# Kernel tuning notes

Measured on AMD Instinct MI355X. Metric: run time of the kernel, lower is better.

Reference implementation:

```python
import jax, jax.numpy as jnp
import numpy as np

N = 100000; E = 1600000; D_IN = 9; HID = 16; HEADS = 8; D = HID * HEADS; G = 1000
NEG_SLOPE = 0.2; LN_EPS = 1e-5


def _gat_conv(x, src, dst, W, a_src, a_dst, b, heads, ch):
    # PyG GATConv (eval mode, self-loops already appended to src/dst)
    h = (x @ W).reshape(-1, heads, ch)                   # [N,H,C]
    al_s = (h * a_src).sum(-1)                           # [N,H]
    al_d = (h * a_dst).sum(-1)                           # [N,H]
    e = al_s[src] + al_d[dst]                            # [Et,H]
    e = jnp.where(e > 0, e, NEG_SLOPE * e)               # LeakyReLU(0.2)
    m = jax.ops.segment_max(e, dst, num_segments=N)      # per-dst softmax
    alpha = jnp.exp(e - m[dst])
    denom = jax.ops.segment_sum(alpha, dst, num_segments=N)
    alpha = alpha / (denom[dst] + 1e-16)
    out = jax.ops.segment_sum(h[src] * alpha[:, :, None], dst, num_segments=N)
    return out.reshape(-1, heads * ch) + b


def _ln_graph(x, g, b):
    # PyG LayerNorm, mode='graph', batch=None: normalize over all nodes+channels
    mu = x.mean()
    var = jnp.mean((x - mu) ** 2)
    return (x - mu) / jnp.sqrt(var + LN_EPS) * g + b


def setup_inputs() -> dict:
    key = jax.random.key(0)
    ks = jax.random.split(key, 20)
    s = 0.1
    p = lambda i, shape: jax.random.normal(ks[i], shape, jnp.float32) * s
    return {
        "x": jax.random.normal(ks[0], (N, D_IN), jnp.float32),
        "edge_index": jax.random.randint(ks[1], (2, E), 0, N),
        "batch": jnp.sort(jax.random.randint(ks[2], (N,), 0, G)),
        "W1": p(3, (D_IN, D)), "a_src1": p(4, (HEADS, HID)), "a_dst1": p(5, (HEADS, HID)), "b1": jnp.zeros((D,), jnp.float32),
        "W2": p(6, (D, D)), "a_src2": p(7, (1, D)), "a_dst2": p(8, (1, D)), "b2": jnp.zeros((D,), jnp.float32),
        "fc1_w": p(9, (D, D)), "fc1_b": jnp.zeros((D,), jnp.float32),
        "fc2_w": p(10, (D, D)), "fc2_b": jnp.zeros((D,), jnp.float32),
        "fc3_w": p(11, (D, D)), "fc3_b": jnp.zeros((D,), jnp.float32),
        "fc4_w": p(12, (D, D)), "fc4_b": jnp.zeros((D,), jnp.float32),
        "g1": jnp.ones((D,), jnp.float32), "beta1": jnp.zeros((D,), jnp.float32),
        "g2": jnp.ones((D,), jnp.float32), "beta2": jnp.zeros((D,), jnp.float32),
        "fcf_w": p(13, (D, 1)), "fcf_b": jnp.zeros((1,), jnp.float32),
    }


def reference(x, edge_index, batch, W1, a_src1, a_dst1, b1, W2, a_src2, a_dst2, b2,
              fc1_w, fc1_b, fc2_w, fc2_b, fc3_w, fc3_b, fc4_w, fc4_b,
              g1, beta1, g2, beta2, fcf_w, fcf_b):
    loops = jnp.arange(N)
    src = jnp.concatenate([edge_index[0], loops])
    dst = jnp.concatenate([edge_index[1], loops])
    h = jax.nn.relu(_gat_conv(x, src, dst, W1, a_src1, a_dst1, b1, HEADS, HID))
    hc = h
    h = jax.nn.relu(h @ fc1_w + fc1_b)
    h = jax.nn.relu(h @ fc2_w + fc2_b + hc)
    h = _ln_graph(h, g1, beta1)
    hc = h
    h = _gat_conv(h, src, dst, W2, a_src2, a_dst2, b2, 1, D)
    h = jax.nn.relu(h @ fc3_w + fc3_b)
    h = h @ fc4_w + fc4_b + hc
    h = _ln_graph(h, g2, beta2)
    h = h @ fcf_w + fcf_b                                # [N,1]
    sums = jax.ops.segment_sum(h, batch, num_segments=G)
    cnt = jax.ops.segment_sum(jnp.ones((N,), h.dtype), batch, num_segments=G)
    return sums / jnp.maximum(cnt, 1.0)[:, None]          # global_mean_pool -> [G,1]
```

## Files before the change

kernel.cpp:

```cpp
#include <hip/hip_runtime.h>
#include <cstdint>

#define NN 100000
#define NE 1600000
#define DI 9
#define DD 128
#define NH 8
#define NG 1000

#define NBK 3125
#define NBLK 256
#define EPB (NE/NBLK)

typedef unsigned int uint;
typedef __attribute__((ext_vector_type(8))) short bf16x8;
typedef __attribute__((ext_vector_type(4))) float f32x4;

__device__ __forceinline__ float leaky(float x){ return x > 0.f ? x : 0.2f*x; }
__device__ __forceinline__ uint f2bf(float f){
  uint u = __float_as_uint(f);
  return (u + 0x7fffu + ((u>>16)&1u)) >> 16;
}
__device__ __forceinline__ float bflo(uint p){ return __uint_as_float(p << 16); }
__device__ __forceinline__ float bfhi(uint p){ return __uint_as_float(p & 0xffff0000u); }
__device__ __forceinline__ uint packbf(float a, float b){ return f2bf(a) | (f2bf(b)<<16); }

union U16 { uint4 u; bf16x8 v; };
__device__ __forceinline__ bf16x8 ld8(const uint* p){ U16 t; t.u = *(const uint4*)p; return t.v; }

__global__ __launch_bounds__(512) void k_hist(const int* __restrict__ dst, int* __restrict__ hist){
  __shared__ int h[NBK];
  for (int i = threadIdx.x; i < NBK; i += 512) h[i] = 0;
  __syncthreads();
  int blk = blockIdx.x;
  int beg = blk*EPB, end = beg + EPB;
  for (int i = beg + threadIdx.x; i < end; i += 512)
    atomicAdd(&h[dst[i] >> 5], 1);
  __syncthreads();
  for (int b = threadIdx.x; b < NBK; b += 512) hist[(size_t)blk*NBK + b] = h[b];
}

__global__ __launch_bounds__(256) void k_bsum(int* __restrict__ hist, int* __restrict__ bsum){
  int b = blockIdx.x*256 + threadIdx.x;
  if (b >= NBK) return;
  int run = 0;
  for (int k = 0; k < NBLK; ++k){
    int t = hist[(size_t)k*NBK + b];
    hist[(size_t)k*NBK + b] = run;
    run += t;
  }
  bsum[b] = run;
}

__global__ __launch_bounds__(1024) void k_bscan(const int* __restrict__ bsum, int* __restrict__ bbase){
  __shared__ int sh[1024];
  __shared__ int carry;
  if (threadIdx.x == 0) carry = 0;
  __syncthreads();
  for (int c0 = 0; c0 < NBK; c0 += 1024){
    int i = c0 + threadIdx.x;
    int v = (i < NBK) ? bsum[i] : 0;
    sh[threadIdx.x] = v;
    __syncthreads();
    for (int off = 1; off < 1024; off <<= 1){
      int t = (threadIdx.x >= off) ? sh[threadIdx.x-off] : 0;
      __syncthreads();
      sh[threadIdx.x] += t;
      __syncthreads();
    }
    if (i < NBK) bbase[i] = carry + sh[threadIdx.x] - v;
    __syncthreads();
    if (threadIdx.x == 0) carry += sh[1023];
    __syncthreads();
  }
}

__global__ __launch_bounds__(512) void k_part(const int* __restrict__ src, const int* __restrict__ dst,
    const int* __restrict__ hist, const int* __restrict__ bbase, uint* __restrict__ ebuf){
  __shared__ int cur[NBK];
  int blk = blockIdx.x;
  for (int b = threadIdx.x; b < NBK; b += 512)
    cur[b] = hist[(size_t)blk*NBK + b] + bbase[b];
  __syncthreads();
  int beg = blk*EPB, end = beg + EPB;
  for (int i = beg + threadIdx.x; i < end; i += 512){
    int d = dst[i], s = src[i];
    int b = d >> 5;
    int p = atomicAdd(&cur[b], 1);
    ebuf[p] = (uint)s | ((uint)(d & 31) << 26);
  }
}

__global__ __launch_bounds__(64) void k_fin(const uint* __restrict__ ebuf, const int* __restrict__ bbase,
    const int* __restrict__ bsum, int* __restrict__ rowptr, int* __restrict__ col){
  __shared__ int cnt32[32];
  __shared__ int exc[32];
  int b = blockIdx.x;
  int lane = threadIdx.x;
  if (lane < 32) cnt32[lane] = 0;
  __syncthreads();
  int base = bbase[b], n = bsum[b];
  for (int i = lane; i < n; i += 64)
    atomicAdd(&cnt32[ebuf[base+i] >> 26], 1);
  __syncthreads();
  if (lane == 0){
    int run = 0;
    for (int d = 0; d < 32; ++d){
      int t = cnt32[d];
      exc[d] = run;
      rowptr[b*32 + d] = base + run;
      run += t;
    }
  }
  __syncthreads();
  if (lane < 32) cnt32[lane] = exc[lane];
  __syncthreads();
  for (int i = lane; i < n; i += 64){
    uint e = ebuf[base+i];
    int d = e >> 26;
    int r = atomicAdd(&cnt32[d], 1);
    col[base + r] = (int)(e & 0x03ffffffu);
  }
  if (b == 0 && lane == 0) rowptr[NN] = NE;
}

__global__ __launch_bounds__(64) void k_wconv5(const float* __restrict__ w0, const float* __restrict__ w1,
    const float* __restrict__ w2, const float* __restrict__ w3, const float* __restrict__ w4,
    uint* __restrict__ o0, uint* __restrict__ o1, uint* __restrict__ o2,
    uint* __restrict__ o3, uint* __restrict__ o4){
  int which = blockIdx.x >> 7;
  int n = blockIdx.x & 127;
  int t = threadIdx.x;
  const float* W = (which==0)?w0:(which==1)?w1:(which==2)?w2:(which==3)?w3:w4;
  uint* WT = (which==0)?o0:(which==1)?o1:(which==2)?o2:(which==3)?o3:o4;
  float a = W[(2*t)*DD + n];
  float b = W[(2*t+1)*DD + n];
  WT[n*64 + t] = packbf(a, b);
}

__global__ __launch_bounds__(128) void k_lin1(const float* __restrict__ x, const float* __restrict__ W1,
    const float* __restrict__ as1, const float* __restrict__ ad1,
    uint* __restrict__ t1b, float* __restrict__ al_s, float* __restrict__ al_d){
  int n = blockIdx.x;
  int c = threadIdx.x;
  const float* xr = x + n*DI;
  float t = 0.f;
  #pragma unroll
  for (int k = 0; k < DI; ++k) t = fmaf(xr[k], W1[k*DD+c], t);
  uint mybf = f2bf(t);
  uint pbf  = (uint)__shfl_xor((int)mybf, 1, 64);
  if (!(c & 1)) t1b[(size_t)n*64 + (c>>1)] = mybf | (pbf<<16);
  float vs = t * as1[c];
  float vd = t * ad1[c];
  #pragma unroll
  for (int m = 8; m >= 1; m >>= 1){ vs += __shfl_xor(vs, m, 16); vd += __shfl_xor(vd, m, 16); }
  if ((c & 15) == 0){
    al_s[n*NH + (c>>4)] = vs;
    al_d[n*NH + (c>>4)] = vd;
  }
}

__global__ __launch_bounds__(256) void k_gat1(const uint* __restrict__ t1b,
    const float* __restrict__ al_s, const float* __restrict__ al_d,
    const int* __restrict__ rowptr, const int* __restrict__ col,
    const float* __restrict__ b1, uint* __restrict__ outb){
  int n = blockIdx.x*4 + (threadIdx.x >> 6);
  if (n >= NN) return;
  uint lane = threadIdx.x & 63;
  uint h = lane >> 3;
  float ald = al_d[(uint)n*NH + h];
  float a0  = __expf(leaky(al_s[(uint)n*NH + h] + ald));
  uint  ps  = t1b[(uint)n*64u + lane];
  float den = a0;
  float s0 = a0*bflo(ps), s1 = a0*bfhi(ps);
  int beg = rowptr[n], end = rowptr[n+1];
  for (int e = beg; e < end; e += 16){
    uint cs[16]; float ls[16]; uint pp[16];
    #pragma unroll
    for (int j = 0; j < 16; ++j){
      int ej = e + j;
      cs[j] = (uint)col[(ej < end) ? ej : (end-1)];
    }
    #pragma unroll
    for (int j = 0; j < 16; ++j){
      ls[j] = al_s[cs[j]*8u + h];
      pp[j] = t1b[cs[j]*64u + lane];
    }
    #pragma unroll
    for (int j = 0; j < 16; ++j){
      float a = (e + j < end) ? __expf(leaky(ls[j] + ald)) : 0.f;
      den += a;
      s0 = fmaf(a, bflo(pp[j]), s0);
      s1 = fmaf(a, bfhi(pp[j]), s1);
    }
  }
  float inv = 1.f/(den + 1e-16f);
  float2 bb = ((const float2*)b1)[lane];
  outb[(uint)n*64u + lane] = packbf(fmaxf(s0*inv + bb.x, 0.f), fmaxf(s1*inv + bb.y, 0.f));
}

__global__ __launch_bounds__(256) void k_gat2(const uint* __restrict__ t2b,
    const float* __restrict__ al_s, const float* __restrict__ al_d,
    const int* __restrict__ rowptr, const int* __restrict__ col,
    const float* __restrict__ b2, uint* __restrict__ outb){
  int n = blockIdx.x*4 + (threadIdx.x >> 6);
  if (n >= NN) return;
  uint lane = threadIdx.x & 63;
  float ald = al_d[n];
  float a0  = __expf(leaky(al_s[n] + ald));
  uint  ps  = t2b[(uint)n*64u + lane];
  float den = a0;
  float s0 = a0*bflo(ps), s1 = a0*bfhi(ps);
  int beg = rowptr[n], end = rowptr[n+1];
  for (int e = beg; e < end; e += 16){
    uint cs[16]; float ls[16]; uint pp[16];
    #pragma unroll
    for (int j = 0; j < 16; ++j){
      int ej = e + j;
      cs[j] = (uint)col[(ej < end) ? ej : (end-1)];
    }
    #pragma unroll
    for (int j = 0; j < 16; ++j){
      ls[j] = al_s[cs[j]];
      pp[j] = t2b[cs[j]*64u + lane];
    }
    #pragma unroll
    for (int j = 0; j < 16; ++j){
      float a = (e + j < end) ? __expf(leaky(ls[j] + ald)) : 0.f;
      den += a;
      s0 = fmaf(a, bflo(pp[j]), s0);
      s1 = fmaf(a, bfhi(pp[j]), s1);
    }
  }
  float inv = 1.f/(den + 1e-16f);
  float2 bb = ((const float2*)b2)[lane];
  outb[(uint)n*64u + lane] = packbf(s0*inv + bb.x, s1*inv + bb.y);
}

template<bool RELU, bool BIAS, bool RES, bool LNRED, bool AL2>
__global__ __launch_bounds__(256) void k_mfma(const uint* __restrict__ Xb, const uint* __restrict__ WTb,
    const float* __restrict__ bias, const uint* __restrict__ resb, uint* __restrict__ outb,
    float* __restrict__ pbuf, const float* __restrict__ avs, const float* __restrict__ avd,
    float* __restrict__ o_als, float* __restrict__ o_ald, int nrows){
  int lane = threadIdx.x & 63;
  int wid  = threadIdx.x >> 6;
  int m0 = blockIdx.x*128 + wid*32;
  int lr = lane & 15, hi4 = lane >> 4;
  f32x4 acc[2][8];
  #pragma unroll
  for (int a = 0; a < 2; ++a)
    #pragma unroll
    for (int c = 0; c < 8; ++c) acc[a][c] = (f32x4){0.f,0.f,0.f,0.f};
  int ra0 = m0 + lr;      if (ra0 > NN-1) ra0 = NN-1;
  int ra1 = m0 + 16 + lr; if (ra1 > NN-1) ra1 = NN-1;
  #pragma unroll
  for (int kk = 0; kk < 4; ++kk){
    int ko = kk*16 + hi4*4;
    bf16x8 a0 = ld8(Xb + (size_t)ra0*64 + ko);
    bf16x8 a1 = ld8(Xb + (size_t)ra1*64 + ko);
    #pragma unroll
    for (int c = 0; c < 8; ++c){
      bf16x8 b = ld8(WTb + (size_t)(c*16 + lr)*64 + ko);
      acc[0][c] = __builtin_amdgcn_mfma_f32_16x16x32_bf16(a0, b, acc[0][c], 0, 0, 0);
      acc[1][c] = __builtin_amdgcn_mfma_f32_16x16x32_bf16(a1, b, acc[1][c], 0, 0, 0);
    }
  }
  if (AL2){
    #pragma unroll
    for (int rg = 0; rg < 2; ++rg){
      #pragma unroll
      for (int r = 0; r < 4; ++r){
        float vs = 0.f, vd = 0.f;
        #pragma unroll
        for (int c = 0; c < 8; ++c){
          float v = acc[rg][c][r];
          vs = fmaf(v, avs[c*16 + lr], vs);
          vd = fmaf(v, avd[c*16 + lr], vd);
        }
        #pragma unroll
        for (int m = 8; m >= 1; m >>= 1){ vs += __shfl_xor(vs, m, 64); vd += __shfl_xor(vd, m, 64); }
        int row = m0 + rg*16 + hi4*4 + r;
        if (lr == 0 && row < nrows){ o_als[row] = vs; o_ald[row] = vd; }
      }
    }
  }
  bool evn = !(lane & 1);
  int cph = lr >> 1;
  float lns = 0.f, lnss = 0.f;
  #pragma unroll
  for (int rg = 0; rg < 2; ++rg){
    #pragma unroll
    for (int c = 0; c < 8; ++c){
      int cp = c*8 + cph;
      #pragma unroll
      for (int r = 0; r < 4; ++r){
        float v0 = acc[rg][c][r];
        float v1 = __shfl_xor(v0, 1, 64);
        int row = m0 + rg*16 + hi4*4 + r;
        if (evn && row < nrows){
          if (BIAS){ float2 bb = ((const float2*)bias)[cp]; v0 += bb.x; v1 += bb.y; }
          if (RES){ uint rr = resb[(size_t)row*64 + cp]; v0 += bflo(rr); v1 += bfhi(rr); }
          if (RELU){ v0 = fmaxf(v0, 0.f); v1 = fmaxf(v1, 0.f); }
          outb[(size_t)row*64 + cp] = packbf(v0, v1);
          if (LNRED){ lns += v0 + v1; lnss += v0*v0 + v1*v1; }
        }
      }
    }
  }
  if (LNRED){
    #pragma unroll
    for (int m = 32; m >= 1; m >>= 1){ lns += __shfl_xor(lns, m, 64); lnss += __shfl_xor(lnss, m, 64); }
    __shared__ float shred[8];
    if (lane == 0){ shred[wid*2] = lns; shred[wid*2+1] = lnss; }
    __syncthreads();
    if (threadIdx.x == 0){
      float S = 0.f, SS = 0.f;
      for (int w = 0; w < 4; ++w){ S += shred[2*w]; SS += shred[2*w+1]; }
      pbuf[blockIdx.x*2] = S; pbuf[blockIdx.x*2+1] = SS;
    }
  }
}

__global__ __launch_bounds__(256) void k_ln_stats(const float* __restrict__ pbuf, float* __restrict__ stats, int nb){
  float s = 0.f, ss = 0.f;
  for (int i = threadIdx.x; i < nb; i += 256){ s += pbuf[2*i]; ss += pbuf[2*i+1]; }
  #pragma unroll
  for (int m = 32; m >= 1; m >>= 1){ s += __shfl_xor(s, m, 64); ss += __shfl_xor(ss, m, 64); }
  __shared__ float sh[8];
  int wid = threadIdx.x >> 6, lane = threadIdx.x & 63;
  if (lane == 0){ sh[wid*2] = s; sh[wid*2+1] = ss; }
  __syncthreads();
  if (threadIdx.x == 0){
    float S = 0.f, SS = 0.f;
    for (int w = 0; w < 4; ++w){ S += sh[2*w]; SS += sh[2*w+1]; }
    const float inv = 1.f/((float)NN*(float)DD);
    float mu = S*inv;
    float var = SS*inv - mu*mu;
    stats[0] = mu;
    stats[1] = rsqrtf(var + 1e-5f);
  }
}

__global__ __launch_bounds__(256) void k_ln_apply_bf(uint* __restrict__ xb, const float* __restrict__ g,
    const float* __restrict__ be, const float* __restrict__ stats){
  const int n4 = NN*16;
  float mu = stats[0], rs = stats[1];
  uint4* x4 = (uint4*)xb;
  const float2* g2 = (const float2*)g;
  const float2* b2 = (const float2*)be;
  for (int i = blockIdx.x*256 + threadIdx.x; i < n4; i += gridDim.x*256){
    int cb = (i & 15)*4;
    uint4 u = x4[i];
    float2 ga = g2[cb],   gb = g2[cb+1], gc = g2[cb+2], gd = g2[cb+3];
    float2 ba = b2[cb],   bb = b2[cb+1], bc = b2[cb+2], bd = b2[cb+3];
    u.x = packbf((bflo(u.x)-mu)*rs*ga.x + ba.x, (bfhi(u.x)-mu)*rs*ga.y + ba.y);
    u.y = packbf((bflo(u.y)-mu)*rs*gb.x + bb.x, (bfhi(u.y)-mu)*rs*gb.y + bb.y);
    u.z = packbf((bflo(u.z)-mu)*rs*gc.x + bc.x, (bfhi(u.z)-mu)*rs*gc.y + bc.y);
    u.w = packbf((bflo(u.w)-mu)*rs*gd.x + bd.x, (bfhi(u.w)-mu)*rs*gd.y + bd.y);
    x4[i] = u;
  }
}

__global__ __launch_bounds__(256) void k_fdot_ln(const uint* __restrict__ xb, const float* __restrict__ g,
    const float* __restrict__ be, const float* __restrict__ stats,
    const float* __restrict__ fw, const float* __restrict__ fb, float* __restrict__ val){
  int n = blockIdx.x*4 + (threadIdx.x >> 6);
  if (n >= NN) return;
  int lane = threadIdx.x & 63;
  float mu = stats[0], rs = stats[1];
  uint p = xb[(size_t)n*64 + lane];
  float2 gg = ((const float2*)g)[lane];
  float2 bb = ((const float2*)be)[lane];
  float2 ww = ((const float2*)fw)[lane];
  float v = ((bflo(p)-mu)*rs*gg.x + bb.x)*ww.x + ((bfhi(p)-mu)*rs*gg.y + bb.y)*ww.y;
  #pragma unroll
  for (int m = 32; m >= 1; m >>= 1) v += __shfl_xor(v, m, 64);
  if (lane == 0) val[n] = v + fb[0];
}

__global__ __launch_bounds__(64) void k_pool(const float* __restrict__ val, const int* __restrict__ batch,
                                             float* __restrict__ out){
  int g = blockIdx.x;
  int lane = threadIdx.x;
  int lo = 0, hi = NN;
  while (lo < hi){ int mid = (lo+hi)>>1; if (batch[mid] < g) lo = mid+1; else hi = mid; }
  int start = lo;
  hi = NN;
  while (lo < hi){ int mid = (lo+hi)>>1; if (batch[mid] < g+1) lo = mid+1; else hi = mid; }
  int end = lo;
  float s = 0.f;
  for (int i = start + lane; i < end; i += 64) s += val[i];
  #pragma unroll
  for (int m = 32; m >= 1; m >>= 1) s += __shfl_xor(s, m, 64);
  if (lane == 0) out[g] = s / fmaxf((float)(end - start), 1.f);
}

extern "C" void kernel_launch(void* const* d_in, const int* in_sizes, int n_in,
                              void* d_out, int out_size, void* d_ws, size_t ws_size,
                              hipStream_t stream){
  const float* x   = (const float*)d_in[0];
  const int*   ei  = (const int*)d_in[1];
  const int* batch = (const int*)d_in[2];
  const float* W1  = (const float*)d_in[3];
  const float* as1 = (const float*)d_in[4];
  const float* ad1 = (const float*)d_in[5];
  const float* b1  = (const float*)d_in[6];
  const float* W2  = (const float*)d_in[7];
  const float* as2 = (const float*)d_in[8];
  const float* ad2 = (const float*)d_in[9];
  const float* b2  = (const float*)d_in[10];
  const float* fc1w= (const float*)d_in[11];
  const float* fc1b= (const float*)d_in[12];
  const float* fc2w= (const float*)d_in[13];
  const float* fc2b= (const float*)d_in[14];
  const float* fc3w= (const float*)d_in[15];
  const float* fc3b= (const float*)d_in[16];
  const float* fc4w= (const float*)d_in[17];
  const float* fc4b= (const float*)d_in[18];
  const float* g1  = (const float*)d_in[19];
  const float* be1 = (const float*)d_in[20];
  const float* g2  = (const float*)d_in[21];
  const float* be2 = (const float*)d_in[22];
  const float* fcw = (const float*)d_in[23];
  const float* fcb = (const float*)d_in[24];
  float* out = (float*)d_out;
  (void)in_sizes; (void)n_in; (void)out_size; (void)ws_size;

  char* ws = (char*)d_ws;
  size_t off = 0;
  auto alloc = [&](size_t bytes)->void*{
    void* p = ws + off;
    off += (bytes + 255) & ~(size_t)255;
    return p;
  };
  float* A    = (float*)alloc((size_t)NN*DD*4);
  float* B    = (float*)alloc((size_t)NN*DD*4);
  float* C    = (float*)alloc((size_t)NN*DD*4);
  float* als1 = (float*)alloc((size_t)NN*NH*4);
  float* ald1 = (float*)alloc((size_t)NN*NH*4);
  float* als2 = (float*)alloc((size_t)NN*4);
  float* ald2 = (float*)alloc((size_t)NN*4);
  float* escr = (float*)alloc((size_t)NE*4);
  int*   rowptr = (int*)alloc((size_t)(NN+1)*4);
  int*   col    = (int*)alloc((size_t)NE*4);
  int*   bsum   = (int*)alloc((size_t)NBK*4);
  int*   bbase  = (int*)alloc((size_t)NBK*4);
  float* pbuf   = (float*)alloc(1024*2*4);
  float* stats  = (float*)alloc(2*4);
  float* val    = (float*)alloc((size_t)NN*4);
  uint* wt_fc1  = (uint*)alloc((size_t)DD*64*4);
  uint* wt_fc2  = (uint*)alloc((size_t)DD*64*4);
  uint* wt_w2   = (uint*)alloc((size_t)DD*64*4);
  uint* wt_fc3  = (uint*)alloc((size_t)DD*64*4);
  uint* wt_fc4  = (uint*)alloc((size_t)DD*64*4);

  uint*  Ab     = (uint*)A;
  uint*  Bb     = (uint*)B;
  uint*  Cb     = (uint*)C;
  int*   hist   = (int*)A;
  uint*  ebuf   = (uint*)escr;

  const int* esrc = ei;
  const int* edst = ei + NE;

  k_hist <<<NBLK, 512, 0, stream>>>(edst, hist);
  k_bsum <<<(NBK+255)/256, 256, 0, stream>>>(hist, bsum);
  k_bscan<<<1, 1024, 0, stream>>>(bsum, bbase);
  k_part <<<NBLK, 512, 0, stream>>>(esrc, edst, hist, bbase, ebuf);
  k_fin  <<<NBK, 64, 0, stream>>>(ebuf, bbase, bsum, rowptr, col);

  k_wconv5<<<5*DD, 64, 0, stream>>>(fc1w, fc2w, W2, fc3w, fc4w,
                                    wt_fc1, wt_fc2, wt_w2, wt_fc3, wt_fc4);

  const int WB = (NN + 3)/4;
  const int GB = (NN + 127)/128;

  k_lin1<<<NN, 128, 0, stream>>>(x, W1, as1, ad1, Ab, als1, ald1);
  k_gat1<<<WB, 256, 0, stream>>>(Ab, als1, ald1, rowptr, col, b1, Bb);

  k_mfma<true,  true, false, false, false><<<GB, 256, 0, stream>>>(Bb, wt_fc1, fc1b, nullptr, Ab, nullptr, nullptr, nullptr, nullptr, nullptr, NN);
  k_mfma<true,  true, true,  true,  false><<<GB, 256, 0, stream>>>(Ab, wt_fc2, fc2b, Bb,      Cb, pbuf,    nullptr, nullptr, nullptr, nullptr, NN);

  k_ln_stats<<<1, 256, 0, stream>>>(pbuf, stats, GB);
  k_ln_apply_bf<<<1024, 256, 0, stream>>>(Cb, g1, be1, stats);

  k_mfma<false, false, false, false, true ><<<GB, 256, 0, stream>>>(Cb, wt_w2, nullptr, nullptr, Ab, nullptr, as2, ad2, als2, ald2, NN);
  k_gat2<<<WB, 256, 0, stream>>>(Ab, als2, ald2, rowptr, col, b2, Bb);

  k_mfma<true,  true, false, false, false><<<GB, 256, 0, stream>>>(Bb, wt_fc3, fc3b, nullptr, Ab, nullptr, nullptr, nullptr, nullptr, nullptr, NN);
  k_mfma<false, true, true,  true,  false><<<GB, 256, 0, stream>>>(Ab, wt_fc4, fc4b, Cb,      Bb, pbuf,    nullptr, nullptr, nullptr, nullptr, NN);

  k_ln_stats<<<1, 256, 0, stream>>>(pbuf, stats, GB);
  k_fdot_ln<<<WB, 256, 0, stream>>>(Bb, g2, be2, stats, fcw, fcb, val);
  k_pool<<<NG, 64, 0, stream>>>(val, batch, out);
}
```

Measured before the change: 476.3 us.

## Use base-2 softmax exponent and lane-parallel edge weights in GAT2 aggregation

Attention logits are pre-scaled by log2(e) when written so both GAT kernels can use exp2f instead of __expf, and LeakyReLU becomes a branch-free fmaxf. In the single-head GAT2 kernel, each lane now loads one neighbour index and computes one edge weight, so 64 edges are handled per step. The weights and indices are then broadcast with readlane, which removes the 64-fold redundant exp and al_s gathers per edge. Column reads are no longer clamped; col gets 64 zeroed padding entries so over-reads past the end stay in bounds, at the cost of an extra memset.

```diff
diff --git a/kernel.cpp b/kernel.cpp
--- a/kernel.cpp
+++ b/kernel.cpp
@@ -7,6 +7,7 @@
 #define DD 128
 #define NH 8
 #define NG 1000
+#define LOG2E 1.44269504f
 
 #define NBK 3125
 #define NBLK 256
@@ -16,7 +17,7 @@
 typedef __attribute__((ext_vector_type(8))) short bf16x8;
 typedef __attribute__((ext_vector_type(4))) float f32x4;
 
-__device__ __forceinline__ float leaky(float x){ return x > 0.f ? x : 0.2f*x; }
+__device__ __forceinline__ float leaky(float x){ return fmaxf(x, 0.2f*x); }
 __device__ __forceinline__ uint f2bf(float f){
   uint u = __float_as_uint(f);
   return (u + 0x7fffu + ((u>>16)&1u)) >> 16;
@@ -24,6 +25,9 @@
 __device__ __forceinline__ float bflo(uint p){ return __uint_as_float(p << 16); }
 __device__ __forceinline__ float bfhi(uint p){ return __uint_as_float(p & 0xffff0000u); }
 __device__ __forceinline__ uint packbf(float a, float b){ return f2bf(a) | (f2bf(b)<<16); }
+__device__ __forceinline__ float rdlanef(float v, int l){
+  return __uint_as_float((uint)__builtin_amdgcn_readlane((int)__float_as_uint(v), l));
+}
 
 union U16 { uint4 u; bf16x8 v; };
 __device__ __forceinline__ bf16x8 ld8(const uint* p){ U16 t; t.u = *(const uint4*)p; return t.v; }
@@ -155,8 +159,8 @@
   #pragma unroll
   for (int m = 8; m >= 1; m >>= 1){ vs += __shfl_xor(vs, m, 16); vd += __shfl_xor(vd, m, 16); }
   if ((c & 15) == 0){
-    al_s[n*NH + (c>>4)] = vs;
-    al_d[n*NH + (c>>4)] = vd;
+    al_s[n*NH + (c>>4)] = vs*LOG2E;
+    al_d[n*NH + (c>>4)] = vd*LOG2E;
   }
 }
 
@@ -169,7 +173,7 @@
   uint lane = threadIdx.x & 63;
   uint h = lane >> 3;
   float ald = al_d[(uint)n*NH + h];
-  float a0  = __expf(leaky(al_s[(uint)n*NH + h] + ald));
+  float a0  = exp2f(leaky(al_s[(uint)n*NH + h] + ald));
   uint  ps  = t1b[(uint)n*64u + lane];
   float den = a0;
   float s0 = a0*bflo(ps), s1 = a0*bfhi(ps);
@@ -177,10 +181,7 @@
   for (int e = beg; e < end; e += 16){
     uint cs[16]; float ls[16]; uint pp[16];
     #pragma unroll
-    for (int j = 0; j < 16; ++j){
-      int ej = e + j;
-      cs[j] = (uint)col[(ej < end) ? ej : (end-1)];
-    }
+    for (int j = 0; j < 16; ++j) cs[j] = (uint)col[e + j];
     #pragma unroll
     for (int j = 0; j < 16; ++j){
       ls[j] = al_s[cs[j]*8u + h];
@@ -188,7 +189,7 @@
     }
     #pragma unroll
     for (int j = 0; j < 16; ++j){
-      float a = (e + j < end) ? __expf(leaky(ls[j] + ald)) : 0.f;
+      float a = (e + j < end) ? exp2f(leaky(ls[j] + ald)) : 0.f;
       den += a;
       s0 = fmaf(a, bflo(pp[j]), s0);
       s1 = fmaf(a, bfhi(pp[j]), s1);
@@ -207,32 +208,36 @@
   if (n >= NN) return;
   uint lane = threadIdx.x & 63;
   float ald = al_d[n];
-  float a0  = __expf(leaky(al_s[n] + ald));
+  float a0  = exp2f(leaky(al_s[n] + ald));
   uint  ps  = t2b[(uint)n*64u + lane];
-  float den = a0;
   float s0 = a0*bflo(ps), s1 = a0*bfhi(ps);
+  float vden = 0.f;
   int beg = rowptr[n], end = rowptr[n+1];
-  for (int e = beg; e < end; e += 16){
-    uint cs[16]; float ls[16]; uint pp[16];
-    #pragma unroll
-    for (int j = 0; j < 16; ++j){
-      int ej = e + j;
-      cs[j] = (uint)col[(ej < end) ? ej : (end-1)];
-    }
-    #pragma unroll
-    for (int j = 0; j < 16; ++j){
-      ls[j] = al_s[cs[j]];
-      pp[j] = t2b[cs[j]*64u + lane];
-    }
-    #pragma unroll
-    for (int j = 0; j < 16; ++j){
-      float a = (e + j < end) ? __expf(leaky(ls[j] + ald)) : 0.f;
-      den += a;
-      s0 = fmaf(a, bflo(pp[j]), s0);
-      s1 = fmaf(a, bfhi(pp[j]), s1);
-    }
-  }
-  float inv = 1.f/(den + 1e-16f);
+  for (int e = beg; e < end; e += 64){
+    int ej = e + (int)lane;
+    uint  mc = (uint)col[ej];
+    float ml = al_s[mc];
+    float ma = (ej < end) ? exp2f(leaky(ml + ald)) : 0.f;
+    vden += ma;
+    int rem = end - e;
+    #pragma unroll
+    for (int jb = 0; jb < 4; ++jb){
+      if (jb*16 < rem){
+        #pragma unroll
+        for (int j = 0; j < 16; ++j){
+          int lsrc = jb*16 + j;
+          float a = rdlanef(ma, lsrc);
+          uint  c = (uint)__builtin_amdgcn_readlane((int)mc, lsrc);
+          uint  p = t2b[c*64u + lane];
+          s0 = fmaf(a, bflo(p), s0);
+          s1 = fmaf(a, bfhi(p), s1);
+        }
+      }
+    }
+  }
+  #pragma unroll
+  for (int m = 32; m >= 1; m >>= 1) vden += __shfl_xor(vden, m, 64);
+  float inv = 1.f/(a0 + vden + 1e-16f);
   float2 bb = ((const float2*)b2)[lane];
   outb[(uint)n*64u + lane] = packbf(s0*inv + bb.x, s1*inv + bb.y);
 }
@@ -280,7 +285,7 @@
         #pragma unroll
         for (int m = 8; m >= 1; m >>= 1){ vs += __shfl_xor(vs, m, 64); vd += __shfl_xor(vd, m, 64); }
         int row = m0 + rg*16 + hi4*4 + r;
-        if (lr == 0 && row < nrows){ o_als[row] = vs; o_ald[row] = vd; }
+        if (lr == 0 && row < nrows){ o_als[row] = vs*LOG2E; o_ald[row] = vd*LOG2E; }
       }
     }
   }
@@ -442,7 +447,7 @@
   float* ald2 = (float*)alloc((size_t)NN*4);
   float* escr = (float*)alloc((size_t)NE*4);
   int*   rowptr = (int*)alloc((size_t)(NN+1)*4);
-  int*   col    = (int*)alloc((size_t)NE*4);
+  int*   col    = (int*)alloc((size_t)(NE+64)*4);
   int*   bsum   = (int*)alloc((size_t)NBK*4);
   int*   bbase  = (int*)alloc((size_t)NBK*4);
   float* pbuf   = (float*)alloc(1024*2*4);
@@ -463,6 +468,8 @@
   const int* esrc = ei;
   const int* edst = ei + NE;
 
+  hipMemsetAsync(col + NE, 0, 64*4, stream);
+
   k_hist <<<NBLK, 512, 0, stream>>>(edst, hist);
   k_bsum <<<(NBK+255)/256, 256, 0, stream>>>(hist, bsum);
   k_bscan<<<1, 1024, 0, stream>>>(bsum, bbase);
```

Result: no change. 477.8 us (+0.3%).
